# Kernel tuning notes

Measured on AMD Instinct MI355X. Metric: run time of the kernel, lower is better.

## Reference

```python
import jax, jax.numpy as jnp
import numpy as np

HID = 1024
HEADS = 16
DH = HID // HEADS
SCALE = DH ** -0.5
L, B = 2048, 2


def setup_inputs() -> dict:
    key = jax.random.key(0)
    ks = jax.random.split(key, 16)
    inp = {
        "query": jax.random.normal(ks[0], (L, B, HID), jnp.float32),
        "key": jax.random.normal(ks[1], (L, B, HID), jnp.float32),
        "value": jax.random.normal(ks[2], (L, B, HID), jnp.float32),
        "mask": jax.random.randint(ks[3], (B, L), 0, 2).astype(bool),
    }
    # xavier-uniform linear weights (torch Linear stores [out, in]; y = x @ W.T + b)
    lim = (6.0 / (HID + HID)) ** 0.5
    for i, name in enumerate(["wq", "wk", "wv", "wfc"]):
        inp[name] = jax.random.uniform(ks[4 + i], (HID, HID), jnp.float32, -lim, lim)
    inp["bq"] = jnp.zeros((HID,), jnp.float32)
    inp["bk"] = jnp.zeros((HID,), jnp.float32)
    inp["bv"] = jnp.zeros((HID,), jnp.float32)
    inp["bfc"] = jnp.zeros((HID,), jnp.float32)
    inp["tao"] = jnp.full((HEADS,), 10.0, jnp.float32)
    return inp


def reference(query, key, value, mask, wq, bq, wk, bk, wv, bv, wfc, bfc, tao):
    # inputs arrive [L, B, D]; module transposes to [B, L, D]
    q = jnp.swapaxes(query, 0, 1)
    k = jnp.swapaxes(key, 0, 1)
    v = jnp.swapaxes(value, 0, 1)
    bsz, length, _ = q.shape

    def heads(x, w, b):
        y = x @ w.T + b                      # [B, L, D]
        return y.reshape(bsz, length, HEADS, DH).transpose(0, 2, 1, 3)  # [B, H, L, d]

    Q = heads(q, wq, bq)
    K = heads(k, wk, bk)
    V = heads(v, wv, bv)

    qk = jnp.einsum("bhqd,bhkd->bhqk", Q, K) * SCALE  # [B, H, L, L]

    # gaussian positional bias: -|i-j|^2/2 * tao_h^-4
    idx = jnp.arange(length, dtype=jnp.float32)
    dist = -0.5 * (idx[:, None] - idx[None, :]) ** 2          # [L, L]
    qk = qk + dist[None, None, :, :] * (tao ** -4)[None, :, None, None]

    qk = jnp.where(mask[:, None, None, :], -jnp.inf, qk)
    attn = jax.nn.softmax(qk, axis=-1)  # dropout is identity in eval mode

    x = jnp.einsum("bhqk,bhkd->bhqd", attn, V)            # [B, H, L, d]
    x = x.transpose(0, 2, 1, 3).reshape(bsz, length, HID)  # [B, L, D]
    x = x @ wfc.T + bfc
    return jnp.swapaxes(x, 0, 1)  # [L, B, D]
```

## Files before the change

kernel.cpp:

```cpp
#include <hip/hip_runtime.h>

#define LQ   2048
#define BQ   2
#define HID  1024
#define NH   16
#define DH   64
#define SCALE 0.125f
#define L2E  1.44269504088896f
#define C1   0.18033688011f
#define EXPOFF 23.0831206542f
#define MASKNEG (-1024.0f)

using short8  = __attribute__((ext_vector_type(8))) short;
using ushort8 = __attribute__((ext_vector_type(8))) unsigned short;
using f32x4   = __attribute__((ext_vector_type(4))) float;
typedef unsigned short u16;
typedef __attribute__((ext_vector_type(2))) __bf16 bf16x2;

__device__ inline u16 f2bf(float x) {
    unsigned int u = __float_as_uint(x);
    u = (u + 0x7fffu + ((u >> 16) & 1u)) >> 16;
    return (u16)u;
}

#if defined(__has_builtin)
#if __has_builtin(__builtin_amdgcn_cvt_pk_bf16_f32)
#define HAVE_PKBF 1
#endif
#if __has_builtin(__builtin_amdgcn_exp2f)
#define HAVE_EXP2 1
#endif
#endif

__device__ inline unsigned int pkbf(float a, float b) {
#ifdef HAVE_PKBF
    bf16x2 r = __builtin_amdgcn_cvt_pk_bf16_f32(a, b);
    return __builtin_bit_cast(unsigned int, r);
#else
    return (unsigned int)f2bf(a) | ((unsigned int)f2bf(b) << 16);
#endif
}

__device__ inline float fexp2(float x) {
#ifdef HAVE_EXP2
    return __builtin_amdgcn_exp2f(x);
#else
    return exp2f(x);
#endif
}

__device__ inline void gl_lds16(const void* g, void* l) {
    __builtin_amdgcn_global_load_lds(
        (const __attribute__((address_space(1))) void*)g,
        (__attribute__((address_space(3))) void*)l, 16, 0, 0);
}

__device__ inline void wvm8() { asm volatile("s_waitcnt vmcnt(8)" ::: "memory"); __builtin_amdgcn_sched_barrier(0); }
__device__ inline void wvm6() { asm volatile("s_waitcnt vmcnt(6)" ::: "memory"); __builtin_amdgcn_sched_barrier(0); }
__device__ inline void wvm4() { asm volatile("s_waitcnt vmcnt(4)" ::: "memory"); __builtin_amdgcn_sched_barrier(0); }
__device__ inline void wvm0() { asm volatile("s_waitcnt vmcnt(0)" ::: "memory"); __builtin_amdgcn_sched_barrier(0); }
__device__ inline void wlg0() { asm volatile("s_waitcnt lgkmcnt(0)" ::: "memory"); __builtin_amdgcn_sched_barrier(0); }
__device__ inline void sbar() {
    __builtin_amdgcn_sched_barrier(0);
    __builtin_amdgcn_s_barrier();
    __builtin_amdgcn_sched_barrier(0);
}

struct CastArgs {
    const float* s[7];
    u16* d[7];
    int n[7];
    const unsigned char* mraw;
    float* mout;
    int mn;
};

__global__ __launch_bounds__(256) void castw(CastArgs a) {
    const int y = blockIdx.y;
    const int t = threadIdx.x;
    if (y == 7) {
        if (blockIdx.x != 0) return;
        __shared__ int cnt;
        if (t == 0) cnt = 0;
        __syncthreads();
        int local = 0;
        for (int i = t; i < a.mn; i += 256)
            if ((i & 3) && a.mraw[i]) local++;
        atomicAdd(&cnt, local);
        __syncthreads();
        bool isInt32 = (cnt == 0);
        const int* mi = (const int*)a.mraw;
        for (int i = t; i < a.mn; i += 256) {
            const bool m = isInt32 ? (mi[i] != 0) : (a.mraw[i] != 0);
            a.mout[i] = m ? (MASKNEG - EXPOFF) : (-EXPOFF);
        }
        return;
    }
    const float* s = a.s[y];
    u16* d = a.d[y];
    const int n4 = a.n[y] >> 2;
    for (int i = blockIdx.x * 256 + t; i < n4; i += gridDim.x * 256) {
        float4 v = *(const float4*)(s + (size_t)i * 4);
        uint2 p;
        p.x = pkbf(v.x, v.y);
        p.y = pkbf(v.z, v.w);
        *(uint2*)(d + (size_t)i * 4) = p;
    }
}

struct QkvArgs {
    const u16* A[3];
    const u16* W[3];
    const float* bias[3];
    u16* out[3];
};

__global__ __launch_bounds__(512) void gemm_qkv(QkvArgs ga) {
    __shared__ u16 As[2][128][64];
    __shared__ u16 Bs[2][128][64];

    const int z = blockIdx.z;
    const u16* A = ga.A[z];
    const u16* W = ga.W[z];
    const float* bias = ga.bias[z];
    u16* outp = ga.out[z];

    const int t = threadIdx.x;
    const int m0 = blockIdx.x * 128;
    const int n0 = blockIdx.y * 128;
    const int lane = t & 63;
    const int lane15 = lane & 15;
    const int quad = lane >> 4;
    const int w = t >> 6;
    const int wm = (w >> 1) * 32;
    const int wn = (w & 1) * 64;

    const int lrow = lane >> 3;
    const int ch = (lane & 7) ^ lrow;
    const u16* aS = A + (size_t)(m0 + 16 * w + lrow) * HID + 8 * ch;
    const u16* bS = W + (size_t)(n0 + 16 * w + lrow) * HID + 8 * ch;

    const int s0 = (quad ^ (lane15 & 7)) * 8;
    const int s1 = ((4 + quad) ^ (lane15 & 7)) * 8;

    f32x4 acc[2][4];
#pragma unroll
    for (int i = 0; i < 2; i++)
#pragma unroll
        for (int j = 0; j < 4; j++) acc[i][j] = (f32x4){0,0,0,0};

#define QKV_STAGE(kt, buf)                                                          \
    {                                                                               \
        _Pragma("unroll")                                                           \
        for (int i = 0; i < 2; i++) {                                               \
            gl_lds16(aS + (size_t)(8 * i) * HID + 64 * (kt), &As[buf][16 * w + 8 * i][0]); \
            gl_lds16(bS + (size_t)(8 * i) * HID + 64 * (kt), &Bs[buf][16 * w + 8 * i][0]); \
        }                                                                           \
    }

    QKV_STAGE(0, 0);
    QKV_STAGE(1, 1);

    for (int kt = 0; kt < 16; ++kt) {
        if (kt < 15) wvm4(); else wvm0();
        sbar();

        const int pb = kt & 1;
        short8 af0[2], af1[2], bf0[4], bf1[4];
#pragma unroll
        for (int i = 0; i < 2; i++) {
            const u16* ar = &As[pb][wm + i * 16 + lane15][0];
            af0[i] = *(const short8*)(ar + s0);
            af1[i] = *(const short8*)(ar + s1);
        }
#pragma unroll
        for (int j = 0; j < 4; j++) {
            const u16* br = &Bs[pb][wn + j * 16 + lane15][0];
            bf0[j] = *(const short8*)(br + s0);
            bf1[j] = *(const short8*)(br + s1);
        }
        wlg0();
        sbar();
        if (kt + 2 < 16) QKV_STAGE(kt + 2, pb);

#pragma unroll
        for (int mi = 0; mi < 2; mi++)
#pragma unroll
            for (int ni = 0; ni < 4; ni++) {
                acc[mi][ni] = __builtin_amdgcn_mfma_f32_16x16x32_bf16(af0[mi], bf0[ni], acc[mi][ni], 0, 0, 0);
                acc[mi][ni] = __builtin_amdgcn_mfma_f32_16x16x32_bf16(af1[mi], bf1[ni], acc[mi][ni], 0, 0, 0);
            }
    }
#undef QKV_STAGE

#pragma unroll
    for (int mi = 0; mi < 2; mi++) {
#pragma unroll
        for (int ni = 0; ni < 4; ni++) {
            const int n = n0 + wn + ni * 16 + lane15;
            const float bv = bias[n];
            const int h = n >> 6, d = n & 63;
#pragma unroll
            for (int r = 0; r < 4; r++) {
                const int m = m0 + wm + mi * 16 + quad * 4 + r;
                const float c = acc[mi][ni][r] + bv;
                const int b = m & 1, l = m >> 1;
                if (z < 2) {
                    outp[(((size_t)(b * NH + h)) * LQ + l) * DH + d] = f2bf(c);
                } else {
                    outp[(((size_t)(b * NH + h)) * DH + d) * LQ + l] = f2bf(c);
                }
            }
        }
    }
}

__global__ __launch_bounds__(256) void gemm_fc(const u16* __restrict__ A,
                                               const u16* __restrict__ W,
                                               const float* __restrict__ bias,
                                               float* __restrict__ outp) {
    __shared__ u16 As[2][128][64];
    __shared__ u16 Bs[2][64][64];

    const int t = threadIdx.x;
    const int m0 = blockIdx.x * 128;
    const int n0 = blockIdx.y * 64;
    const int lane = t & 63;
    const int lane15 = lane & 15;
    const int quad = lane >> 4;
    const int w = t >> 6;
    const int wm = (w >> 1) * 64;
    const int wn = (w & 1) * 32;

    const int lrow = lane >> 3;
    const int ch = (lane & 7) ^ ((lane >> 3) & 7);
    const u16* aS = A + (size_t)(m0 + 32 * w + lrow) * HID + 8 * ch;
    const u16* bS = W + (size_t)(n0 + 16 * w + lrow) * HID + 8 * ch;

    const int s0 = (quad ^ (lane15 & 7)) * 8;
    const int s1 = ((4 + quad) ^ (lane15 & 7)) * 8;

    f32x4 acc[4][2];
#pragma unroll
    for (int i = 0; i < 4; i++)
#pragma unroll
        for (int j = 0; j < 2; j++) acc[i][j] = (f32x4){0,0,0,0};

#define FC_STAGE(kt, buf)                                                           \
    {                                                                               \
        _Pragma("unroll")                                                           \
        for (int i = 0; i < 4; i++)                                                 \
            gl_lds16(aS + (size_t)(8 * i) * HID + 64 * (kt), &As[buf][32 * w + 8 * i][0]); \
        _Pragma("unroll")                                                           \
        for (int i = 0; i < 2; i++)                                                 \
            gl_lds16(bS + (size_t)(8 * i) * HID + 64 * (kt), &Bs[buf][16 * w + 8 * i][0]); \
    }

    FC_STAGE(0, 0);
    FC_STAGE(1, 1);

    for (int kt = 0; kt < 16; ++kt) {
        if (kt < 15) wvm6(); else wvm0();
        sbar();

        const int pb = kt & 1;
        short8 af0[4], af1[4], bf0[2], bf1[2];
#pragma unroll
        for (int i = 0; i < 4; i++) {
            const u16* ar = &As[pb][wm + i * 16 + lane15][0];
            af0[i] = *(const short8*)(ar + s0);
            af1[i] = *(const short8*)(ar + s1);
        }
#pragma unroll
        for (int j = 0; j < 2; j++) {
            const u16* br = &Bs[pb][wn + j * 16 + lane15][0];
            bf0[j] = *(const short8*)(br + s0);
            bf1[j] = *(const short8*)(br + s1);
        }
        wlg0();
        sbar();
        if (kt + 2 < 16) FC_STAGE(kt + 2, pb);

#pragma unroll
        for (int mi = 0; mi < 4; mi++)
#pragma unroll
            for (int ni = 0; ni < 2; ni++) {
                acc[mi][ni] = __builtin_amdgcn_mfma_f32_16x16x32_bf16(af0[mi], bf0[ni], acc[mi][ni], 0, 0, 0);
                acc[mi][ni] = __builtin_amdgcn_mfma_f32_16x16x32_bf16(af1[mi], bf1[ni], acc[mi][ni], 0, 0, 0);
            }
    }
#undef FC_STAGE

#pragma unroll
    for (int mi = 0; mi < 4; mi++) {
#pragma unroll
        for (int ni = 0; ni < 2; ni++) {
            const int n = n0 + wn + ni * 16 + lane15;
            const float bv = bias[n];
#pragma unroll
            for (int r = 0; r < 4; r++) {
                const int m = m0 + wm + mi * 16 + quad * 4 + r;
                outp[(size_t)m * HID + n] = acc[mi][ni][r] + bv;
            }
        }
    }
}

#define PSTR 72

__global__ __launch_bounds__(256, 2) void attn_kernel(const u16* __restrict__ Qg,
                                                      const u16* __restrict__ Kg,
                                                      const u16* __restrict__ Vtg,
                                                      const float* __restrict__ maskF,
                                                      const float* __restrict__ tao,
                                                      u16* __restrict__ Xa) {
    __shared__ u16 Ks[2][64][64];
    __shared__ u16 Vt[2][64][64];
    __shared__ u16 PT[128][PSTR];
    __shared__ float smaskL[LQ];

    const int bh = blockIdx.x;
    const int q0 = blockIdx.y * 128;
    const int b = bh >> 4;
    const int h = bh & 15;
    const int t = threadIdx.x;
    const int w = t >> 6;
    const int lane = t & 63;
    const int lane15 = lane & 15;
    const int quad = lane >> 4;

    const u16* Kbase = Kg + (size_t)bh * LQ * DH;
    const u16* Vtbase = Vtg + (size_t)bh * DH * LQ;
    const float* mrow = maskF + b * LQ;

    const float tv = tao[h];
    const float t2 = tv * tv;
    const float nb = -0.5f / (t2 * t2);
    const float nb2 = nb * L2E;
    const float sqn = sqrtf(-nb2);
    const float R = sqrtf(-40.0f / nb2) + 1.0f;

    int c_lo = (int)floorf(((float)q0 - R) * (1.0f / 64.0f));
    int c_hi = (int)floorf(((float)(q0 + 127) + R) * (1.0f / 64.0f));
    if (c_lo < 0) c_lo = 0;
    if (c_hi > (LQ / 64 - 1)) c_hi = LQ / 64 - 1;
    if (c_hi < c_lo) c_hi = c_lo;
    const int c1 = (c_lo + 1 <= c_hi) ? (c_lo + 1) : c_hi;

    const int lr = lane >> 3;
    const int sch = (lane & 7) ^ lr;
    const u16* kS0 = Kbase + (size_t)(16 * w + lr) * DH + 8 * sch;
    const u16* kS1 = Kbase + (size_t)(16 * w + 8 + lr) * DH + 8 * sch;
    const u16* vS0 = Vtbase + (size_t)(16 * w + lr) * LQ + 8 * sch;
    const u16* vS1 = Vtbase + (size_t)(16 * w + 8 + lr) * LQ + 8 * sch;

#define ATT_STAGE(cc, buf)                                             \
    {                                                                  \
        gl_lds16(kS0 + (size_t)(cc) * (64 * DH), &Ks[buf][16 * w][0]); \
        gl_lds16(kS1 + (size_t)(cc) * (64 * DH), &Ks[buf][16 * w + 8][0]); \
        gl_lds16(vS0 + 64 * (cc), &Vt[buf][16 * w][0]);                \
        gl_lds16(vS1 + 64 * (cc), &Vt[buf][16 * w + 8][0]);            \
    }

    const int qrow0 = q0 + w * 32 + lane15;
    const int qrow1 = qrow0 + 16;
    short8 qA00, qA01, qA10, qA11;
    {
        const u16* qp0 = Qg + ((size_t)bh * LQ + qrow0) * DH + quad * 8;
        qA00 = *(const short8*)(qp0);
        qA01 = *(const short8*)(qp0 + 32);
        const u16* qp1 = Qg + ((size_t)bh * LQ + qrow1) * DH + quad * 8;
        qA10 = *(const short8*)(qp1);
        qA11 = *(const short8*)(qp1 + 32);
    }
    const float4 mT0 = *(const float4*)(mrow + 4 * t);
    const float4 mT1 = *(const float4*)(mrow + 1024 + 4 * t);
    __builtin_amdgcn_sched_barrier(0);
    ATT_STAGE(c_lo, 0);
    ATT_STAGE(c1, 1);
    __builtin_amdgcn_sched_barrier(0);
    *(float4*)&smaskL[4 * t] = mT0;
    *(float4*)&smaskL[1024 + 4 * t] = mT1;
    wlg0();

    const int s0 = (quad ^ (lane15 & 7)) * 8;
    const int s1 = ((4 + quad) ^ (lane15 & 7)) * 8;

    float crs[16];
#pragma unroll
    for (int i = 0; i < 16; i++)
        crs[i] = (float)((i >> 2) * 16 + (i & 3)) * sqn;

    short8 ones;
#pragma unroll
    for (int i = 0; i < 8; i++) ones[i] = (short)0x3F80;

    f32x4 O0[4], O1[4];
#pragma unroll
    for (int mt = 0; mt < 4; mt++) { O0[mt] = (f32x4){0,0,0,0}; O1[mt] = (f32x4){0,0,0,0}; }
    f32x4 Lac0 = (f32x4){0,0,0,0};
    f32x4 Lac1 = (f32x4){0,0,0,0};

    const float eb00 = (float)(qrow0 - quad * 4);
    const float eb01 = (float)(qrow1 - quad * 4);
    const int prow0 = w * 32 + lane15;
    const int prow1 = prow0 + 16;

    for (int c = c_lo; c <= c_hi; ++c) {
        if (c < c_hi) wvm4(); else wvm0();
        sbar();

        const int pb = (c - c_lo) & 1;

        short8 ka[4], kb[4], va[4], vb[4];
#pragma unroll
        for (int kt = 0; kt < 4; kt++) {
            const u16* kr = &Ks[pb][kt * 16 + lane15][0];
            ka[kt] = *(const short8*)(kr + s0);
            kb[kt] = *(const short8*)(kr + s1);
            const u16* vr = &Vt[pb][kt * 16 + lane15][0];
            va[kt] = *(const short8*)(vr + s0);
            vb[kt] = *(const short8*)(vr + s1);
        }

        f32x4 S0[4], S1[4];
#pragma unroll
        for (int kt = 0; kt < 4; kt++) {
            S0[kt] = __builtin_amdgcn_mfma_f32_16x16x32_bf16(ka[kt], qA00, (f32x4){0,0,0,0}, 0, 0, 0);
            S0[kt] = __builtin_amdgcn_mfma_f32_16x16x32_bf16(kb[kt], qA01, S0[kt], 0, 0, 0);
            S1[kt] = __builtin_amdgcn_mfma_f32_16x16x32_bf16(ka[kt], qA10, (f32x4){0,0,0,0}, 0, 0, 0);
            S1[kt] = __builtin_amdgcn_mfma_f32_16x16x32_bf16(kb[kt], qA11, S1[kt], 0, 0, 0);
        }

        wlg0();
        sbar();
        if (c + 2 <= c_hi) ATT_STAGE(c + 2, pb);

        float4 mv[4];
#pragma unroll
        for (int kt = 0; kt < 4; kt++)
            mv[kt] = *(const float4*)&smaskL[64 * c + kt * 16 + quad * 4];

        const float ebS0 = (eb00 - (float)(64 * c)) * sqn;
        const float ebS1 = (eb01 - (float)(64 * c)) * sqn;
#pragma unroll
        for (int kt = 0; kt < 4; kt++) {
            float pr0[4], pr1[4];
#pragma unroll
            for (int r = 0; r < 4; r++) {
                const float mb = ((const float*)&mv[kt])[r];
                const float dp0 = ebS0 - crs[kt * 4 + r];
                const float dp1 = ebS1 - crs[kt * 4 + r];
                pr0[r] = fexp2(fmaf(S0[kt][r], C1, fmaf(-dp0, dp0, mb)));
                pr1[r] = fexp2(fmaf(S1[kt][r], C1, fmaf(-dp1, dp1, mb)));
            }
            uint2 pk0, pk1;
            pk0.x = pkbf(pr0[0], pr0[1]);
            pk0.y = pkbf(pr0[2], pr0[3]);
            pk1.x = pkbf(pr1[0], pr1[1]);
            pk1.y = pkbf(pr1[2], pr1[3]);
            *(uint2*)&PT[prow0][kt * 16 + quad * 4] = pk0;
            *(uint2*)&PT[prow1][kt * 16 + quad * 4] = pk1;
        }

        const short8 pB00 = *(const short8*)&PT[prow0][quad * 8];
        const short8 pB01 = *(const short8*)&PT[prow0][32 + quad * 8];
        const short8 pB10 = *(const short8*)&PT[prow1][quad * 8];
        const short8 pB11 = *(const short8*)&PT[prow1][32 + quad * 8];
        Lac0 = __builtin_amdgcn_mfma_f32_16x16x32_bf16(ones, pB00, Lac0, 0, 0, 0);
        Lac0 = __builtin_amdgcn_mfma_f32_16x16x32_bf16(ones, pB01, Lac0, 0, 0, 0);
        Lac1 = __builtin_amdgcn_mfma_f32_16x16x32_bf16(ones, pB10, Lac1, 0, 0, 0);
        Lac1 = __builtin_amdgcn_mfma_f32_16x16x32_bf16(ones, pB11, Lac1, 0, 0, 0);

#pragma unroll
        for (int mt = 0; mt < 4; mt++) {
            O0[mt] = __builtin_amdgcn_mfma_f32_16x16x32_bf16(va[mt], pB00, O0[mt], 0, 0, 0);
            O0[mt] = __builtin_amdgcn_mfma_f32_16x16x32_bf16(vb[mt], pB01, O0[mt], 0, 0, 0);
            O1[mt] = __builtin_amdgcn_mfma_f32_16x16x32_bf16(va[mt], pB10, O1[mt], 0, 0, 0);
            O1[mt] = __builtin_amdgcn_mfma_f32_16x16x32_bf16(vb[mt], pB11, O1[mt], 0, 0, 0);
        }
    }
#undef ATT_STAGE

    {
        const float inv0 = 1.0f / Lac0[0];
        u16* dst0 = Xa + ((size_t)qrow0 * BQ + b) * HID + h * DH;
#pragma unroll
        for (int mt = 0; mt < 4; mt++) {
            uint2 pk2;
            pk2.x = pkbf(O0[mt][0] * inv0, O0[mt][1] * inv0);
            pk2.y = pkbf(O0[mt][2] * inv0, O0[mt][3] * inv0);
            *(uint2*)(dst0 + mt * 16 + quad * 4) = pk2;
        }
        const float inv1 = 1.0f / Lac1[0];
        u16* dst1 = Xa + ((size_t)qrow1 * BQ + b) * HID + h * DH;
#pragma unroll
        for (int mt = 0; mt < 4; mt++) {
            uint2 pk2;
            pk2.x = pkbf(O1[mt][0] * inv1, O1[mt][1] * inv1);
            pk2.y = pkbf(O1[mt][2] * inv1, O1[mt][3] * inv1);
            *(uint2*)(dst1 + mt * 16 + quad * 4) = pk2;
        }
    }
}

extern "C" void kernel_launch(void* const* d_in, const int* in_sizes, int n_in,
                              void* d_out, int out_size, void* d_ws, size_t ws_size,
                              hipStream_t stream) {
    const float* q    = (const float*)d_in[0];
    const float* k    = (const float*)d_in[1];
    const float* v    = (const float*)d_in[2];
    const void*  mask = d_in[3];
    const float* wq   = (const float*)d_in[4];
    const float* wk   = (const float*)d_in[5];
    const float* wv   = (const float*)d_in[6];
    const float* wfc  = (const float*)d_in[7];
    const float* bq   = (const float*)d_in[8];
    const float* bk   = (const float*)d_in[9];
    const float* bv   = (const float*)d_in[10];
    const float* bfc  = (const float*)d_in[11];
    const float* tao  = (const float*)d_in[12];

    const size_t NE = (size_t)LQ * BQ * HID;
    const size_t NW = (size_t)HID * HID;
    u16* base = (u16*)d_ws;
    u16* Qp    = base;
    u16* Kp    = base + NE;
    u16* Vtp   = base + 2 * NE;
    u16* Xa    = base + 3 * NE;
    u16* qbf   = base + 4 * NE;
    u16* kbf   = base + 5 * NE;
    u16* vbf   = base + 6 * NE;
    u16* wqbf  = base + 7 * NE;
    u16* wkbf  = wqbf + NW;
    u16* wvbf  = wkbf + NW;
    u16* wfcbf = wvbf + NW;
    float* maskF = (float*)(wfcbf + NW);

    CastArgs ca;
    ca.s[0] = q;   ca.d[0] = qbf;   ca.n[0] = (int)NE;
    ca.s[1] = k;   ca.d[1] = kbf;   ca.n[1] = (int)NE;
    ca.s[2] = v;   ca.d[2] = vbf;   ca.n[2] = (int)NE;
    ca.s[3] = wq;  ca.d[3] = wqbf;  ca.n[3] = (int)NW;
    ca.s[4] = wk;  ca.d[4] = wkbf;  ca.n[4] = (int)NW;
    ca.s[5] = wv;  ca.d[5] = wvbf;  ca.n[5] = (int)NW;
    ca.s[6] = wfc; ca.d[6] = wfcbf; ca.n[6] = (int)NW;
    ca.mraw = (const unsigned char*)mask;
    ca.mout = maskF;
    ca.mn = BQ * LQ;
    castw<<<dim3(256, 8), 256, 0, stream>>>(ca);

    QkvArgs ga;
    ga.A[0] = qbf;  ga.W[0] = wqbf;  ga.bias[0] = bq;  ga.out[0] = Qp;
    ga.A[1] = kbf;  ga.W[1] = wkbf;  ga.bias[1] = bk;  ga.out[1] = Kp;
    ga.A[2] = vbf;  ga.W[2] = wvbf;  ga.bias[2] = bv;  ga.out[2] = Vtp;
    gemm_qkv<<<dim3(32, 8, 3), 512, 0, stream>>>(ga);

    attn_kernel<<<dim3(32, 16), 256, 0, stream>>>(Qp, Kp, Vtp, maskF, tao, Xa);

    gemm_fc<<<dim3(32, 16), 256, 0, stream>>>(Xa, wfcbf, bfc, (float*)d_out);
}
```

Baseline: 223.8 us.

## Split attention block across 8 waves with 16 query rows per wave

```diff
diff --git a/kernel.cpp b/kernel.cpp
--- a/kernel.cpp
+++ b/kernel.cpp
@@ -58,6 +58,7 @@
 __device__ inline void wvm8() { asm volatile("s_waitcnt vmcnt(8)" ::: "memory"); __builtin_amdgcn_sched_barrier(0); }
 __device__ inline void wvm6() { asm volatile("s_waitcnt vmcnt(6)" ::: "memory"); __builtin_amdgcn_sched_barrier(0); }
 __device__ inline void wvm4() { asm volatile("s_waitcnt vmcnt(4)" ::: "memory"); __builtin_amdgcn_sched_barrier(0); }
+__device__ inline void wvm2() { asm volatile("s_waitcnt vmcnt(2)" ::: "memory"); __builtin_amdgcn_sched_barrier(0); }
 __device__ inline void wvm0() { asm volatile("s_waitcnt vmcnt(0)" ::: "memory"); __builtin_amdgcn_sched_barrier(0); }
 __device__ inline void wlg0() { asm volatile("s_waitcnt lgkmcnt(0)" ::: "memory"); __builtin_amdgcn_sched_barrier(0); }
 __device__ inline void sbar() {
@@ -308,7 +309,7 @@
 
 #define PSTR 72
 
-__global__ __launch_bounds__(256, 2) void attn_kernel(const u16* __restrict__ Qg,
+__global__ __launch_bounds__(512, 4) void attn_kernel(const u16* __restrict__ Qg,
                                                       const u16* __restrict__ Kg,
                                                       const u16* __restrict__ Vtg,
                                                       const float* __restrict__ maskF,
@@ -349,157 +350,107 @@
 
     const int lr = lane >> 3;
     const int sch = (lane & 7) ^ lr;
-    const u16* kS0 = Kbase + (size_t)(16 * w + lr) * DH + 8 * sch;
-    const u16* kS1 = Kbase + (size_t)(16 * w + 8 + lr) * DH + 8 * sch;
-    const u16* vS0 = Vtbase + (size_t)(16 * w + lr) * LQ + 8 * sch;
-    const u16* vS1 = Vtbase + (size_t)(16 * w + 8 + lr) * LQ + 8 * sch;
-
-#define ATT_STAGE(cc, buf)                                             \
-    {                                                                  \
-        gl_lds16(kS0 + (size_t)(cc) * (64 * DH), &Ks[buf][16 * w][0]); \
-        gl_lds16(kS1 + (size_t)(cc) * (64 * DH), &Ks[buf][16 * w + 8][0]); \
-        gl_lds16(vS0 + 64 * (cc), &Vt[buf][16 * w][0]);                \
-        gl_lds16(vS1 + 64 * (cc), &Vt[buf][16 * w + 8][0]);            \
-    }
-
-    const int qrow0 = q0 + w * 32 + lane15;
-    const int qrow1 = qrow0 + 16;
-    short8 qA00, qA01, qA10, qA11;
+    const u16* kS = Kbase + (size_t)(8 * w + lr) * DH + 8 * sch;
+    const u16* vS = Vtbase + (size_t)(8 * w + lr) * LQ + 8 * sch;
+
+#define ATT_STAGE(cc, buf)                                            \
+    {                                                                 \
+        gl_lds16(kS + (size_t)(cc) * (64 * DH), &Ks[buf][8 * w][0]);  \
+        gl_lds16(vS + 64 * (cc), &Vt[buf][8 * w][0]);                 \
+    }
+
+    const int qrow = q0 + w * 16 + lane15;
+    short8 qA0, qA1;
     {
-        const u16* qp0 = Qg + ((size_t)bh * LQ + qrow0) * DH + quad * 8;
-        qA00 = *(const short8*)(qp0);
-        qA01 = *(const short8*)(qp0 + 32);
-        const u16* qp1 = Qg + ((size_t)bh * LQ + qrow1) * DH + quad * 8;
-        qA10 = *(const short8*)(qp1);
-        qA11 = *(const short8*)(qp1 + 32);
-    }
-    const float4 mT0 = *(const float4*)(mrow + 4 * t);
-    const float4 mT1 = *(const float4*)(mrow + 1024 + 4 * t);
+        const u16* qp_ = Qg + ((size_t)bh * LQ + qrow) * DH + quad * 8;
+        qA0 = *(const short8*)(qp_);
+        qA1 = *(const short8*)(qp_ + 32);
+    }
+    const float4 mT = *(const float4*)(mrow + 4 * t);
     __builtin_amdgcn_sched_barrier(0);
     ATT_STAGE(c_lo, 0);
     ATT_STAGE(c1, 1);
     __builtin_amdgcn_sched_barrier(0);
-    *(float4*)&smaskL[4 * t] = mT0;
-    *(float4*)&smaskL[1024 + 4 * t] = mT1;
+    *(float4*)&smaskL[4 * t] = mT;
     wlg0();
 
     const int s0 = (quad ^ (lane15 & 7)) * 8;
     const int s1 = ((4 + quad) ^ (lane15 & 7)) * 8;
 
-    float crs[16];
-#pragma unroll
-    for (int i = 0; i < 16; i++)
-        crs[i] = (float)((i >> 2) * 16 + (i & 3)) * sqn;
-
     short8 ones;
 #pragma unroll
     for (int i = 0; i < 8; i++) ones[i] = (short)0x3F80;
 
-    f32x4 O0[4], O1[4];
-#pragma unroll
-    for (int mt = 0; mt < 4; mt++) { O0[mt] = (f32x4){0,0,0,0}; O1[mt] = (f32x4){0,0,0,0}; }
-    f32x4 Lac0 = (f32x4){0,0,0,0};
-    f32x4 Lac1 = (f32x4){0,0,0,0};
-
-    const float eb00 = (float)(qrow0 - quad * 4);
-    const float eb01 = (float)(qrow1 - quad * 4);
-    const int prow0 = w * 32 + lane15;
-    const int prow1 = prow0 + 16;
+    f32x4 O[4];
+#pragma unroll
+    for (int mt = 0; mt < 4; mt++) O[mt] = (f32x4){0,0,0,0};
+    f32x4 Lac = (f32x4){0,0,0,0};
+
+    const float eb0 = (float)(qrow - quad * 4);
+    const int prow = w * 16 + lane15;
 
     for (int c = c_lo; c <= c_hi; ++c) {
-        if (c < c_hi) wvm4(); else wvm0();
+        if (c < c_hi) wvm2(); else wvm0();
         sbar();
 
         const int pb = (c - c_lo) & 1;
 
-        short8 ka[4], kb[4], va[4], vb[4];
+        f32x4 S[4];
 #pragma unroll
         for (int kt = 0; kt < 4; kt++) {
             const u16* kr = &Ks[pb][kt * 16 + lane15][0];
-            ka[kt] = *(const short8*)(kr + s0);
-            kb[kt] = *(const short8*)(kr + s1);
-            const u16* vr = &Vt[pb][kt * 16 + lane15][0];
-            va[kt] = *(const short8*)(vr + s0);
-            vb[kt] = *(const short8*)(vr + s1);
-        }
-
-        f32x4 S0[4], S1[4];
+            const short8 ka = *(const short8*)(kr + s0);
+            const short8 kb = *(const short8*)(kr + s1);
+            S[kt] = __builtin_amdgcn_mfma_f32_16x16x32_bf16(ka, qA0, (f32x4){0,0,0,0}, 0, 0, 0);
+            S[kt] = __builtin_amdgcn_mfma_f32_16x16x32_bf16(kb, qA1, S[kt], 0, 0, 0);
+        }
+
+        const float ebS = (eb0 - (float)(64 * c)) * sqn;
 #pragma unroll
         for (int kt = 0; kt < 4; kt++) {
-            S0[kt] = __builtin_amdgcn_mfma_f32_16x16x32_bf16(ka[kt], qA00, (f32x4){0,0,0,0}, 0, 0, 0);
-            S0[kt] = __builtin_amdgcn_mfma_f32_16x16x32_bf16(kb[kt], qA01, S0[kt], 0, 0, 0);
-            S1[kt] = __builtin_amdgcn_mfma_f32_16x16x32_bf16(ka[kt], qA10, (f32x4){0,0,0,0}, 0, 0, 0);
-            S1[kt] = __builtin_amdgcn_mfma_f32_16x16x32_bf16(kb[kt], qA11, S1[kt], 0, 0, 0);
+            const float4 mv = *(const float4*)&smaskL[64 * c + kt * 16 + quad * 4];
+            float pr[4];
+#pragma unroll
+            for (int r = 0; r < 4; r++) {
+                const float dp = ebS - (float)(kt * 16 + r) * sqn;
+                const float tb = fmaf(-dp, dp, ((const float*)&mv)[r]);
+                pr[r] = fexp2(fmaf(S[kt][r], C1, tb));
+            }
+            uint2 pk2;
+            pk2.x = pkbf(pr[0], pr[1]);
+            pk2.y = pkbf(pr[2], pr[3]);
+            *(uint2*)&PT[prow][kt * 16 + quad * 4] = pk2;
+        }
+
+        const short8 pB0 = *(const short8*)&PT[prow][quad * 8];
+        const short8 pB1 = *(const short8*)&PT[prow][32 + quad * 8];
+        Lac = __builtin_amdgcn_mfma_f32_16x16x32_bf16(ones, pB0, Lac, 0, 0, 0);
+        Lac = __builtin_amdgcn_mfma_f32_16x16x32_bf16(ones, pB1, Lac, 0, 0, 0);
+
+#pragma unroll
+        for (int mt = 0; mt < 4; mt++) {
+            const u16* vr = &Vt[pb][mt * 16 + lane15][0];
+            const short8 va = *(const short8*)(vr + s0);
+            const short8 vb = *(const short8*)(vr + s1);
+            O[mt] = __builtin_amdgcn_mfma_f32_16x16x32_bf16(va, pB0, O[mt], 0, 0, 0);
+            O[mt] = __builtin_amdgcn_mfma_f32_16x16x32_bf16(vb, pB1, O[mt], 0, 0, 0);
         }
 
         wlg0();
         sbar();
         if (c + 2 <= c_hi) ATT_STAGE(c + 2, pb);
-
-        float4 mv[4];
-#pragma unroll
-        for (int kt = 0; kt < 4; kt++)
-            mv[kt] = *(const float4*)&smaskL[64 * c + kt * 16 + quad * 4];
-
-        const float ebS0 = (eb00 - (float)(64 * c)) * sqn;
-        const float ebS1 = (eb01 - (float)(64 * c)) * sqn;
-#pragma unroll
-        for (int kt = 0; kt < 4; kt++) {
-            float pr0[4], pr1[4];
-#pragma unroll
-            for (int r = 0; r < 4; r++) {
-                const float mb = ((const float*)&mv[kt])[r];
-                const float dp0 = ebS0 - crs[kt * 4 + r];
-                const float dp1 = ebS1 - crs[kt * 4 + r];
-                pr0[r] = fexp2(fmaf(S0[kt][r], C1, fmaf(-dp0, dp0, mb)));
-                pr1[r] = fexp2(fmaf(S1[kt][r], C1, fmaf(-dp1, dp1, mb)));
-            }
-            uint2 pk0, pk1;
-            pk0.x = pkbf(pr0[0], pr0[1]);
-            pk0.y = pkbf(pr0[2], pr0[3]);
-            pk1.x = pkbf(pr1[0], pr1[1]);
-            pk1.y = pkbf(pr1[2], pr1[3]);
-            *(uint2*)&PT[prow0][kt * 16 + quad * 4] = pk0;
-            *(uint2*)&PT[prow1][kt * 16 + quad * 4] = pk1;
-        }
-
-        const short8 pB00 = *(const short8*)&PT[prow0][quad * 8];
-        const short8 pB01 = *(const short8*)&PT[prow0][32 + quad * 8];
-        const short8 pB10 = *(const short8*)&PT[prow1][quad * 8];
-        const short8 pB11 = *(const short8*)&PT[prow1][32 + quad * 8];
-        Lac0 = __builtin_amdgcn_mfma_f32_16x16x32_bf16(ones, pB00, Lac0, 0, 0, 0);
-        Lac0 = __builtin_amdgcn_mfma_f32_16x16x32_bf16(ones, pB01, Lac0, 0, 0, 0);
-        Lac1 = __builtin_amdgcn_mfma_f32_16x16x32_bf16(ones, pB10, Lac1, 0, 0, 0);
-        Lac1 = __builtin_amdgcn_mfma_f32_16x16x32_bf16(ones, pB11, Lac1, 0, 0, 0);
-
-#pragma unroll
-        for (int mt = 0; mt < 4; mt++) {
-            O0[mt] = __builtin_amdgcn_mfma_f32_16x16x32_bf16(va[mt], pB00, O0[mt], 0, 0, 0);
-            O0[mt] = __builtin_amdgcn_mfma_f32_16x16x32_bf16(vb[mt], pB01, O0[mt], 0, 0, 0);
-            O1[mt] = __builtin_amdgcn_mfma_f32_16x16x32_bf16(va[mt], pB10, O1[mt], 0, 0, 0);
-            O1[mt] = __builtin_amdgcn_mfma_f32_16x16x32_bf16(vb[mt], pB11, O1[mt], 0, 0, 0);
-        }
     }
 #undef ATT_STAGE
 
     {
-        const float inv0 = 1.0f / Lac0[0];
-        u16* dst0 = Xa + ((size_t)qrow0 * BQ + b) * HID + h * DH;
+        const float inv = 1.0f / Lac[0];
+        u16* dst = Xa + ((size_t)qrow * BQ + b) * HID + h * DH;
 #pragma unroll
         for (int mt = 0; mt < 4; mt++) {
             uint2 pk2;
-            pk2.x = pkbf(O0[mt][0] * inv0, O0[mt][1] * inv0);
-            pk2.y = pkbf(O0[mt][2] * inv0, O0[mt][3] * inv0);
-            *(uint2*)(dst0 + mt * 16 + quad * 4) = pk2;
-        }
-        const float inv1 = 1.0f / Lac1[0];
-        u16* dst1 = Xa + ((size_t)qrow1 * BQ + b) * HID + h * DH;
-#pragma unroll
-        for (int mt = 0; mt < 4; mt++) {
-            uint2 pk2;
-            pk2.x = pkbf(O1[mt][0] * inv1, O1[mt][1] * inv1);
-            pk2.y = pkbf(O1[mt][2] * inv1, O1[mt][3] * inv1);
-            *(uint2*)(dst1 + mt * 16 + quad * 4) = pk2;
+            pk2.x = pkbf(O[mt][0] * inv, O[mt][1] * inv);
+            pk2.y = pkbf(O[mt][2] * inv, O[mt][3] * inv);
+            *(uint2*)(dst + mt * 16 + quad * 4) = pk2;
         }
     }
 }
@@ -556,7 +507,7 @@
     ga.A[2] = vbf;  ga.W[2] = wvbf;  ga.bias[2] = bv;  ga.out[2] = Vtp;
     gemm_qkv<<<dim3(32, 8, 3), 512, 0, stream>>>(ga);
 
-    attn_kernel<<<dim3(32, 16), 256, 0, stream>>>(Qp, Kp, Vtp, maskF, tao, Xa);
+    attn_kernel<<<dim3(32, 16), 512, 0, stream>>>(Qp, Kp, Vtp, maskF, tao, Xa);
 
     gemm_fc<<<dim3(32, 16), 256, 0, stream>>>(Xa, wfcbf, bfc, (float*)d_out);
 }
```

Result: no change. 223.4 us (-0.2%).
